# Optimization experiments

Measured on AMD Instinct MI355X. Metric: run time of the kernel, lower is better.

## Reference

```python
import jax, jax.numpy as jnp
import numpy as np

NEG_SLOPE = 0.2  # DenseGATConv default negative_slope


def _add_self_loops(adj):
    n = adj.shape[-1]
    idx = jnp.arange(n)
    return adj.at[:, idx, idx].set(1.0)


def dense_gat_conv(x, adj, W, att_src, att_dst, bias, concat):
    """PyG DenseGATConv forward (eval mode, add_loop=True).
    x: [B,N,F], adj: [B,N,N] (0/1), W: [F,H*C], att_*: [H,C], bias: [H*C] or [C]."""
    B, N, _ = x.shape
    H, C = att_src.shape
    h = (x @ W).reshape(B, N, H, C)                     # projected features
    a_src = jnp.einsum('bnhc,hc->bnh', h, att_src)      # [B,N,H]
    a_dst = jnp.einsum('bnhc,hc->bnh', h, att_dst)      # [B,N,H]
    # alpha[b,i,j,h] = a_src[b,j,h] + a_dst[b,i,h]
    alpha = a_src[:, None, :, :] + a_dst[:, :, None, :]  # [B,N,N,H]
    alpha = jax.nn.leaky_relu(alpha, NEG_SLOPE)
    adj = _add_self_loops(adj)
    alpha = jnp.where(adj[..., None] == 0, -jnp.inf, alpha)
    alpha = jax.nn.softmax(alpha, axis=2)               # softmax over sources j
    out = jnp.einsum('bijh,bjhc->bihc', alpha, h)       # [B,N,H,C]
    out = out.reshape(B, N, H * C) if concat else out.mean(axis=2)
    return out + bias


def setup_inputs() -> dict:
    key = jax.random.key(0)
    ks = jax.random.split(key, 10)
    B, N, F, H, C, NC = 1, 4096, 512, 8, 64, 16
    x = jax.random.normal(ks[0], (B, N, F), dtype=jnp.float32)
    adj = (jax.random.uniform(ks[1], (B, N, N)) < 0.01).astype(jnp.float32)
    s1 = 1.0 / np.sqrt(F)
    s2 = 1.0 / np.sqrt(H * C)
    return {
        'x': x,
        'adj': adj,
        'W1': jax.random.normal(ks[2], (F, H * C), dtype=jnp.float32) * s1,
        'att_src1': jax.random.normal(ks[3], (H, C), dtype=jnp.float32) * s1,
        'att_dst1': jax.random.normal(ks[4], (H, C), dtype=jnp.float32) * s1,
        'b1': jnp.zeros((H * C,), dtype=jnp.float32),
        'W2': jax.random.normal(ks[5], (H * C, NC), dtype=jnp.float32) * s2,
        'att_src2': jax.random.normal(ks[6], (1, NC), dtype=jnp.float32) * s2,
        'att_dst2': jax.random.normal(ks[7], (1, NC), dtype=jnp.float32) * s2,
        'b2': jnp.zeros((NC,), dtype=jnp.float32),
    }


def reference(x, adj, W1, att_src1, att_dst1, b1, W2, att_src2, att_dst2, b2):
    # eval mode: all dropout(p=0.6) layers are identity
    h = dense_gat_conv(x, adj, W1, att_src1, att_dst1, b1, concat=True)
    h = jax.nn.elu(h)
    out = dense_gat_conv(h, adj, W2, att_src2, att_dst2, b2, concat=False)
    return out
```

## Files before the change

### kernel.cpp

```cpp
#include <hip/hip_runtime.h>
#include <hip/hip_bf16.h>
#include <hip/hip_fp16.h>

#define N_NODES 4096
#define F_IN    512
#define HC      512
#define H_HEADS 8
#define C_DIM   64
#define NCLS    16
#define CAP     192
#define NEG_SLOPE 0.2f

typedef __bf16 bf16x8 __attribute__((ext_vector_type(8)));
typedef float  f32x4  __attribute__((ext_vector_type(4)));
typedef unsigned short us8 __attribute__((ext_vector_type(8)));


#define XBLKS 1024
#define WBLKS 64

__global__ __launch_bounds__(256) void k_prep(const float* __restrict__ x,
                                              const float* __restrict__ W,
                                              const float* __restrict__ adj,
                                              ushort* __restrict__ xhi,
                                              ushort* __restrict__ xlo,
                                              ushort* __restrict__ whiT,
                                              ushort* __restrict__ wloT,
                                              int* __restrict__ row_cnt,
                                              int* __restrict__ col_idx) {
    __shared__ float tile[64][65];
    __shared__ int cnt_s;
    int b = blockIdx.x;
    int t = threadIdx.x;
    if (b < XBLKS) {
        int tid = b * 256 + t;
        int rg = tid >> 9;
        rg = tid >> 10;
        int c  = tid & 1023;
        int kb = c >> 6;
        int l  = c & 63;
        int row = rg * 16 + (l & 15);
        int kbase = kb * 32 + (l >> 4) * 8;
        const float* src = &x[(size_t)row * F_IN + kbase];
        float4 v0 = *(const float4*)&src[0];
        float4 v1 = *(const float4*)&src[4];
        float f[8] = {v0.x, v0.y, v0.z, v0.w, v1.x, v1.y, v1.z, v1.w};
        us8 hv, lv;
#pragma unroll
        for (int u = 0; u < 8; ++u) {
            __bf16 h = (__bf16)f[u];
            __bf16 lo_ = (__bf16)(f[u] - (float)h);
            hv[u] = __builtin_bit_cast(unsigned short, h);
            lv[u] = __builtin_bit_cast(unsigned short, lo_);
        }
        *(us8*)&xhi[(size_t)tid * 8] = hv;
        *(us8*)&xlo[(size_t)tid * 8] = lv;
    } else if (b < XBLKS + WBLKS) {
        int bb = b - XBLKS;
        int n0 = (bb & 7) * 64, k0 = (bb >> 3) * 64;
#pragma unroll
        for (int i = 0; i < 4; ++i) {
            int r = i * 16 + (t >> 4);
            int c = (t & 15) * 4;
            *(float4*)&tile[r][c] = *(const float4*)&W[(size_t)(k0 + r) * HC + n0 + c];
        }
        __syncthreads();
        int rg_local = t >> 6;
        int l = t & 63;
        int n_local = rg_local * 16 + (l & 15);
#pragma unroll
        for (int kb_local = 0; kb_local < 2; ++kb_local) {
            int k_local = kb_local * 32 + (l >> 4) * 8;
            us8 hv, lv;
#pragma unroll
            for (int u = 0; u < 8; ++u) {
                float f = tile[k_local + u][n_local];
                __bf16 h = (__bf16)f;
                __bf16 lo_ = (__bf16)(f - (float)h);
                hv[u] = __builtin_bit_cast(unsigned short, h);
                lv[u] = __builtin_bit_cast(unsigned short, lo_);
            }
            int rg = (n0 >> 4) + rg_local;
            int kb = (k0 >> 5) + kb_local;
            size_t off = ((size_t)(rg * 16 + kb) * 64 + l) * 8;
            *(us8*)&whiT[off] = hv;
            *(us8*)&wloT[off] = lv;
        }
    } else {
        int i = b - (XBLKS + WBLKS);
        if (t == 0) cnt_s = 0;
        __syncthreads();
        const float4* row = (const float4*)(adj + (size_t)i * N_NODES);
        int* cols = col_idx + (size_t)i * CAP;
#pragma unroll
        for (int it = 0; it < 4; ++it) {
            int idx4 = it * 256 + t;
            float4 v = row[idx4];
            int j0 = idx4 * 4;
            if (v.x != 0.f && j0 + 0 != i) { int p = atomicAdd(&cnt_s, 1); if (p < CAP - 1) cols[p] = j0 + 0; }
            if (v.y != 0.f && j0 + 1 != i) { int p = atomicAdd(&cnt_s, 1); if (p < CAP - 1) cols[p] = j0 + 1; }
            if (v.z != 0.f && j0 + 2 != i) { int p = atomicAdd(&cnt_s, 1); if (p < CAP - 1) cols[p] = j0 + 2; }
            if (v.w != 0.f && j0 + 3 != i) { int p = atomicAdd(&cnt_s, 1); if (p < CAP - 1) cols[p] = j0 + 3; }
        }
        __syncthreads();
        if (t == 0) {
            int p = min(cnt_s, CAP - 1);
            cols[p] = i;
            row_cnt[i] = p + 1;
        }
    }
}

__global__ __launch_bounds__(256) void k_gemm1(const ushort* __restrict__ Ahi,
                                               const ushort* __restrict__ Alo,
                                               const ushort* __restrict__ Bhi,
                                               const ushort* __restrict__ Blo,
                                               const float* __restrict__ att_src,
                                               const float* __restrict__ att_dst,
                                               __half* __restrict__ C,
                                               float* __restrict__ a_src,
                                               float* __restrict__ a_dst) {
    __shared__ __align__(16) ushort smem[4][2048];
    __shared__ float s_s[2][64], s_d[2][64];
    int t = threadIdx.x;
    int w = t >> 6, lane = t & 63;
    int n0 = blockIdx.x * 64;
    int m0 = blockIdx.y * 64;
    const ushort* src = (w == 0) ? Ahi : (w == 1) ? Alo : (w == 2) ? Bhi : Blo;
    int rg0 = ((w < 2) ? m0 : n0) >> 4;
    int mw = (w & 1) * 32, nw = (w >> 1) * 32;
    f32x4 acc[2][2] = {};
    for (int kb = 0; kb < 16; ++kb) {
#pragma unroll
        for (int g = 0; g < 4; ++g) {
            const ushort* gp = src + ((size_t)((rg0 + g) * 16 + kb) * 64 + lane) * 8;
            __builtin_amdgcn_global_load_lds(
                (const __attribute__((address_space(1))) void*)gp,
                (__attribute__((address_space(3))) void*)&smem[w][g * 512],
                16, 0, 0);
        }
        __syncthreads();
        bf16x8 ahi[2], alo[2], bhi[2], blo[2];
#pragma unroll
        for (int mi = 0; mi < 2; ++mi) {
            int g = (mw >> 4) + mi;
            ahi[mi] = __builtin_bit_cast(bf16x8, *(const us8*)&smem[0][g * 512 + lane * 8]);
            alo[mi] = __builtin_bit_cast(bf16x8, *(const us8*)&smem[1][g * 512 + lane * 8]);
        }
#pragma unroll
        for (int ni = 0; ni < 2; ++ni) {
            int g = (nw >> 4) + ni;
            bhi[ni] = __builtin_bit_cast(bf16x8, *(const us8*)&smem[2][g * 512 + lane * 8]);
            blo[ni] = __builtin_bit_cast(bf16x8, *(const us8*)&smem[3][g * 512 + lane * 8]);
        }
#pragma unroll
        for (int mi = 0; mi < 2; ++mi)
#pragma unroll
            for (int ni = 0; ni < 2; ++ni) {
                acc[mi][ni] = __builtin_amdgcn_mfma_f32_16x16x32_bf16(ahi[mi], bhi[ni], acc[mi][ni], 0, 0, 0);
                acc[mi][ni] = __builtin_amdgcn_mfma_f32_16x16x32_bf16(alo[mi], bhi[ni], acc[mi][ni], 0, 0, 0);
                acc[mi][ni] = __builtin_amdgcn_mfma_f32_16x16x32_bf16(ahi[mi], blo[ni], acc[mi][ni], 0, 0, 0);
            }
        __syncthreads();
    }
    int r0 = (lane >> 4) * 4;
    int cn = lane & 15;
    float as0 = att_src[n0 + nw + cn],      as1 = att_src[n0 + nw + 16 + cn];
    float ad0 = att_dst[n0 + nw + cn],      ad1 = att_dst[n0 + nw + 16 + cn];
#pragma unroll
    for (int mi = 0; mi < 2; ++mi)
#pragma unroll
        for (int r = 0; r < 4; ++r) {
            float ps = acc[mi][0][r] * as0 + acc[mi][1][r] * as1;
            float pd = acc[mi][0][r] * ad0 + acc[mi][1][r] * ad1;
#pragma unroll
            for (int o = 1; o < 16; o <<= 1) {
                ps += __shfl_xor(ps, o, 64);
                pd += __shfl_xor(pd, o, 64);
            }
            if (cn == 0) {
                int row = mw + mi * 16 + r0 + r;
                s_s[w >> 1][row] = ps;
                s_d[w >> 1][row] = pd;
            }
        }
#pragma unroll
    for (int mi = 0; mi < 2; ++mi)
#pragma unroll
        for (int ni = 0; ni < 2; ++ni) {
            size_t base = (size_t)(m0 + mw + mi * 16 + r0) * HC + (n0 + nw + ni * 16 + cn);
#pragma unroll
            for (int r = 0; r < 4; ++r)
                C[base + (size_t)r * HC] = __float2half(acc[mi][ni][r]);
        }
    __syncthreads();
    if (t < 64) {
        a_src[(m0 + t) * H_HEADS + blockIdx.x] = s_s[0][t] + s_s[1][t];
        a_dst[(m0 + t) * H_HEADS + blockIdx.x] = s_d[0][t] + s_d[1][t];
    }
}

__global__ __launch_bounds__(256) void k_agg1(const __half* __restrict__ hf,
                                              const float* __restrict__ a_src,
                                              const float* __restrict__ a_dst,
                                              const int* __restrict__ row_cnt,
                                              const int* __restrict__ col_idx,
                                              const float* __restrict__ b1,
                                              __half* __restrict__ elu1) {
    int i = blockIdx.x;
    int t = threadIdx.x;
    __shared__ float wL[CAP][H_HEADS];
    __shared__ int   colL[CAP];
    __shared__ float denom[H_HEADS];
    __shared__ float ad[H_HEADS];
    int cnt = row_cnt[i];
    if (t < H_HEADS) ad[t] = a_dst[i * H_HEADS + t];
    for (int j = t; j < cnt; j += 256) colL[j] = col_idx[(size_t)i * CAP + j];
    __syncthreads();
    for (int idx = t; idx < cnt * H_HEADS; idx += 256) {
        int j = idx >> 3, h = idx & 7;
        float l = a_src[colL[j] * H_HEADS + h] + ad[h];
        l = (l > 0.f) ? l : NEG_SLOPE * l;
        wL[j][h] = __expf(l);
    }
    __syncthreads();
    {
        int h = t >> 5, l32 = t & 31;
        float s = 0.f;
        for (int j = l32; j < cnt; j += 32) s += wL[j][h];
#pragma unroll
        for (int o = 16; o > 0; o >>= 1) s += __shfl_down(s, o, 32);
        if (l32 == 0) denom[h] = s;
    }
    __syncthreads();
    int e = t * 2;
    int h = e >> 6;
    float ax = 0.f, ay = 0.f;
    int j = 0;
    for (; j + 4 <= cnt; j += 4) {
        int c0 = colL[j], c1 = colL[j + 1], c2 = colL[j + 2], c3 = colL[j + 3];
        float2 v0 = __half22float2(*(const __half2*)&hf[(size_t)c0 * HC + e]);
        float2 v1 = __half22float2(*(const __half2*)&hf[(size_t)c1 * HC + e]);
        float2 v2 = __half22float2(*(const __half2*)&hf[(size_t)c2 * HC + e]);
        float2 v3 = __half22float2(*(const __half2*)&hf[(size_t)c3 * HC + e]);
        float w0 = wL[j][h], w1 = wL[j + 1][h], w2 = wL[j + 2][h], w3 = wL[j + 3][h];
        ax += w0 * v0.x + w1 * v1.x + w2 * v2.x + w3 * v3.x;
        ay += w0 * v0.y + w1 * v1.y + w2 * v2.y + w3 * v3.y;
    }
    for (; j < cnt; ++j) {
        int c0 = colL[j];
        float2 v0 = __half22float2(*(const __half2*)&hf[(size_t)c0 * HC + e]);
        float w0 = wL[j][h];
        ax += w0 * v0.x;
        ay += w0 * v0.y;
    }
    float inv = 1.f / denom[h];
    float o0 = ax * inv + b1[e];
    float o1 = ay * inv + b1[e + 1];
    o0 = (o0 > 0.f) ? o0 : (__expf(o0) - 1.f);
    o1 = (o1 > 0.f) ? o1 : (__expf(o1) - 1.f);
    *(__half2*)&elu1[(size_t)i * HC + e] = __floats2half2_rn(o0, o1);
}

__global__ __launch_bounds__(256) void k_gemm2(const __half* __restrict__ elu1,
                                               const float* __restrict__ W2,
                                               const float* __restrict__ att_src2,
                                               const float* __restrict__ att_dst2,
                                               float* __restrict__ h2,
                                               float* __restrict__ a_src2,
                                               float* __restrict__ a_dst2) {
    __shared__ float W2s[HC * NCLS];
    __shared__ float h2s[16][NCLS];
    int t = threadIdx.x;
    int n0 = blockIdx.x * 16;
#pragma unroll
    for (int u = 0; u < 8; ++u) {
        int idx = (u * 256 + t) * 4;
        *(float4*)&W2s[idx] = *(const float4*)&W2[idx];
    }
    __syncthreads();
    int nl = t >> 4, c = t & 15;
    const __half2* row = (const __half2*)(elu1 + (size_t)(n0 + nl) * HC);
    float acc = 0.f;
    for (int k = 0; k < HC; k += 4) {
        float2 v0 = __half22float2(row[k >> 1]);
        float2 v1 = __half22float2(row[(k >> 1) + 1]);
        acc += v0.x * W2s[(k + 0) * NCLS + c] + v0.y * W2s[(k + 1) * NCLS + c]
             + v1.x * W2s[(k + 2) * NCLS + c] + v1.y * W2s[(k + 3) * NCLS + c];
    }
    h2[(size_t)(n0 + nl) * NCLS + c] = acc;
    h2s[nl][c] = acc;
    __syncthreads();
    if (t < 16) {
        float s = 0.f, d = 0.f;
#pragma unroll
        for (int cc = 0; cc < NCLS; ++cc) {
            s += h2s[t][cc] * att_src2[cc];
            d += h2s[t][cc] * att_dst2[cc];
        }
        a_src2[n0 + t] = s;
        a_dst2[n0 + t] = d;
    }
}

__global__ __launch_bounds__(256) void k_agg2(const float* __restrict__ h2,
                                              const float* __restrict__ a_src2,
                                              const float* __restrict__ a_dst2,
                                              const int* __restrict__ row_cnt,
                                              const int* __restrict__ col_idx,
                                              const float* __restrict__ b2,
                                              float* __restrict__ out) {
    int t = threadIdx.x;
    int w = t >> 6, lane = t & 63;
    int i = blockIdx.x * 4 + w;
    __shared__ float ew[4][CAP];
    __shared__ int   colL[4][CAP];
    int cnt = row_cnt[i];
    float adi = a_dst2[i];
    float sum = 0.f;
    for (int j = lane; j < cnt; j += 64) {
        int col = col_idx[(size_t)i * CAP + j];
        colL[w][j] = col;
        float l = a_src2[col] + adi;
        l = (l > 0.f) ? l : NEG_SLOPE * l;
        float e = __expf(l);
        ew[w][j] = e;
        sum += e;
    }
#pragma unroll
    for (int o = 32; o > 0; o >>= 1) sum += __shfl_xor(sum, o, 64);
    int q = lane >> 4, c = lane & 15;
    float acc = 0.f;
    for (int j = q; j < cnt; j += 4)
        acc += ew[w][j] * h2[(size_t)colL[w][j] * NCLS + c];
    acc += __shfl_down(acc, 32, 64);
    acc += __shfl_down(acc, 16, 64);
    if (lane < NCLS)
        out[(size_t)i * NCLS + lane] = acc / sum + b2[lane];
}

extern "C" void kernel_launch(void* const* d_in, const int* in_sizes, int n_in,
                              void* d_out, int out_size, void* d_ws, size_t ws_size,
                              hipStream_t stream) {
    const float* x        = (const float*)d_in[0];
    const float* adj      = (const float*)d_in[1];
    const float* W1       = (const float*)d_in[2];
    const float* att_src1 = (const float*)d_in[3];
    const float* att_dst1 = (const float*)d_in[4];
    const float* b1       = (const float*)d_in[5];
    const float* W2       = (const float*)d_in[6];
    const float* att_src2 = (const float*)d_in[7];
    const float* att_dst2 = (const float*)d_in[8];
    const float* b2       = (const float*)d_in[9];
    float* out = (float*)d_out;

    char* ws = (char*)d_ws;
    int*    row_cnt = (int*)ws;     ws += (size_t)N_NODES * 4;
    int*    col_idx = (int*)ws;     ws += (size_t)N_NODES * CAP * 4;
    __half* h1f     = (__half*)ws;  ws += (size_t)N_NODES * HC * 2;
    float*  a_src   = (float*)ws;   ws += (size_t)N_NODES * H_HEADS * 4;
    float*  a_dst   = (float*)ws;   ws += (size_t)N_NODES * H_HEADS * 4;
    __half* elu1    = (__half*)ws;  ws += (size_t)N_NODES * HC * 2;
    float*  h2      = (float*)ws;   ws += (size_t)N_NODES * NCLS * 4;
    float*  as2     = (float*)ws;   ws += (size_t)N_NODES * 4;
    float*  ad2     = (float*)ws;   ws += (size_t)N_NODES * 4;
    ushort* x_hi    = (ushort*)ws;  ws += (size_t)N_NODES * F_IN * 2;
    ushort* x_lo    = (ushort*)ws;  ws += (size_t)N_NODES * F_IN * 2;
    ushort* w_hiT   = (ushort*)ws;  ws += (size_t)F_IN * HC * 2;
    ushort* w_loT   = (ushort*)ws;  ws += (size_t)F_IN * HC * 2;

    hipLaunchKernelGGL(k_prep, dim3(XBLKS + WBLKS + N_NODES), dim3(256), 0, stream,
                       x, W1, adj, x_hi, x_lo, w_hiT, w_loT, row_cnt, col_idx);
    hipLaunchKernelGGL(k_gemm1, dim3(HC / 64, N_NODES / 64), dim3(256), 0, stream,
                       x_hi, x_lo, w_hiT, w_loT, att_src1, att_dst1, h1f, a_src, a_dst);
    hipLaunchKernelGGL(k_agg1, dim3(N_NODES), dim3(256), 0, stream,
                       h1f, a_src, a_dst, row_cnt, col_idx, b1, elu1);
    hipLaunchKernelGGL(k_gemm2, dim3(N_NODES / 16), dim3(256), 0, stream,
                       elu1, W2, att_src2, att_dst2, h2, as2, ad2);
    hipLaunchKernelGGL(k_agg2, dim3(N_NODES / 4), dim3(256), 0, stream,
                       h2, as2, ad2, row_cnt, col_idx, b2, out);
}
```

Baseline: 165.5 us.

## Fuse second-layer projection into aggregation and overlap adjacency scan with GEMM1

Moves the adjacency-to-CSR scan out of the prep kernel into extra blocks of the first GEMM launch, so the adjacency read runs alongside the projection GEMM. Fuses the second linear projection and its attention logits into the first aggregation kernel. Each node's ELU output now stays in shared memory and is multiplied by W2 there, which removes the elu1 round trip through global memory and one kernel launch. In exchange, each aggregation block reads W2 directly from global memory (cached) and adds two block barriers and a small reduction.

```diff
diff --git a/kernel.cpp b/kernel.cpp
--- a/kernel.cpp
+++ b/kernel.cpp
@@ -18,24 +18,20 @@
 
 #define XBLKS 1024
 #define WBLKS 64
-
-__global__ __launch_bounds__(256) void k_prep(const float* __restrict__ x,
-                                              const float* __restrict__ W,
-                                              const float* __restrict__ adj,
-                                              ushort* __restrict__ xhi,
-                                              ushort* __restrict__ xlo,
-                                              ushort* __restrict__ whiT,
-                                              ushort* __restrict__ wloT,
-                                              int* __restrict__ row_cnt,
-                                              int* __restrict__ col_idx) {
+#define GBLKS 512
+
+__global__ __launch_bounds__(256) void k_split(const float* __restrict__ x,
+                                               const float* __restrict__ W,
+                                               ushort* __restrict__ xhi,
+                                               ushort* __restrict__ xlo,
+                                               ushort* __restrict__ whiT,
+                                               ushort* __restrict__ wloT) {
     __shared__ float tile[64][65];
-    __shared__ int cnt_s;
     int b = blockIdx.x;
     int t = threadIdx.x;
     if (b < XBLKS) {
         int tid = b * 256 + t;
-        int rg = tid >> 9;
-        rg = tid >> 10;
+        int rg = tid >> 10;
         int c  = tid & 1023;
         int kb = c >> 6;
         int l  = c & 63;
@@ -55,7 +51,7 @@
         }
         *(us8*)&xhi[(size_t)tid * 8] = hv;
         *(us8*)&xlo[(size_t)tid * 8] = lv;
-    } else if (b < XBLKS + WBLKS) {
+    } else {
         int bb = b - XBLKS;
         int n0 = (bb & 7) * 64, k0 = (bb >> 3) * 64;
 #pragma unroll
@@ -86,8 +82,28 @@
             *(us8*)&whiT[off] = hv;
             *(us8*)&wloT[off] = lv;
         }
-    } else {
-        int i = b - (XBLKS + WBLKS);
+    }
+}
+
+__global__ __launch_bounds__(256) void k_gemm1(const ushort* __restrict__ Ahi,
+                                               const ushort* __restrict__ Alo,
+                                               const ushort* __restrict__ Bhi,
+                                               const ushort* __restrict__ Blo,
+                                               const float* __restrict__ att_src,
+                                               const float* __restrict__ att_dst,
+                                               const float* __restrict__ adj,
+                                               __half* __restrict__ C,
+                                               float* __restrict__ a_src,
+                                               float* __restrict__ a_dst,
+                                               int* __restrict__ row_cnt,
+                                               int* __restrict__ col_idx) {
+    __shared__ __align__(16) ushort smem[4][2048];
+    __shared__ float s_s[2][64], s_d[2][64];
+    __shared__ int cnt_s;
+    int b = blockIdx.x;
+    int t = threadIdx.x;
+    if (b >= GBLKS) {
+        int i = b - GBLKS;
         if (t == 0) cnt_s = 0;
         __syncthreads();
         const float4* row = (const float4*)(adj + (size_t)i * N_NODES);
@@ -108,24 +124,12 @@
             cols[p] = i;
             row_cnt[i] = p + 1;
         }
-    }
-}
-
-__global__ __launch_bounds__(256) void k_gemm1(const ushort* __restrict__ Ahi,
-                                               const ushort* __restrict__ Alo,
-                                               const ushort* __restrict__ Bhi,
-                                               const ushort* __restrict__ Blo,
-                                               const float* __restrict__ att_src,
-                                               const float* __restrict__ att_dst,
-                                               __half* __restrict__ C,
-                                               float* __restrict__ a_src,
-                                               float* __restrict__ a_dst) {
-    __shared__ __align__(16) ushort smem[4][2048];
-    __shared__ float s_s[2][64], s_d[2][64];
-    int t = threadIdx.x;
+        return;
+    }
     int w = t >> 6, lane = t & 63;
-    int n0 = blockIdx.x * 64;
-    int m0 = blockIdx.y * 64;
+    int head = b & 7;
+    int n0 = head * 64;
+    int m0 = (b >> 3) * 64;
     const ushort* src = (w == 0) ? Ahi : (w == 1) ? Alo : (w == 2) ? Bhi : Blo;
     int rg0 = ((w < 2) ? m0 : n0) >> 4;
     int mw = (w & 1) * 32, nw = (w >> 1) * 32;
@@ -195,8 +199,8 @@
         }
     __syncthreads();
     if (t < 64) {
-        a_src[(m0 + t) * H_HEADS + blockIdx.x] = s_s[0][t] + s_s[1][t];
-        a_dst[(m0 + t) * H_HEADS + blockIdx.x] = s_d[0][t] + s_d[1][t];
+        a_src[(m0 + t) * H_HEADS + head] = s_s[0][t] + s_s[1][t];
+        a_dst[(m0 + t) * H_HEADS + head] = s_d[0][t] + s_d[1][t];
     }
 }
 
@@ -206,13 +210,20 @@
                                               const int* __restrict__ row_cnt,
                                               const int* __restrict__ col_idx,
                                               const float* __restrict__ b1,
-                                              __half* __restrict__ elu1) {
+                                              const float* __restrict__ W2,
+                                              const float* __restrict__ att_src2,
+                                              const float* __restrict__ att_dst2,
+                                              float* __restrict__ h2,
+                                              float* __restrict__ a_src2,
+                                              float* __restrict__ a_dst2) {
     int i = blockIdx.x;
     int t = threadIdx.x;
     __shared__ float wL[CAP][H_HEADS];
     __shared__ int   colL[CAP];
     __shared__ float denom[H_HEADS];
     __shared__ float ad[H_HEADS];
+    __shared__ float elu_s[HC];
+    __shared__ float part[16][17];
     int cnt = row_cnt[i];
     if (t < H_HEADS) ad[t] = a_dst[i * H_HEADS + t];
     for (int j = t; j < cnt; j += 256) colL[j] = col_idx[(size_t)i * CAP + j];
@@ -259,47 +270,29 @@
     float o1 = ay * inv + b1[e + 1];
     o0 = (o0 > 0.f) ? o0 : (__expf(o0) - 1.f);
     o1 = (o1 > 0.f) ? o1 : (__expf(o1) - 1.f);
-    *(__half2*)&elu1[(size_t)i * HC + e] = __floats2half2_rn(o0, o1);
-}
-
-__global__ __launch_bounds__(256) void k_gemm2(const __half* __restrict__ elu1,
-                                               const float* __restrict__ W2,
-                                               const float* __restrict__ att_src2,
-                                               const float* __restrict__ att_dst2,
-                                               float* __restrict__ h2,
-                                               float* __restrict__ a_src2,
-                                               float* __restrict__ a_dst2) {
-    __shared__ float W2s[HC * NCLS];
-    __shared__ float h2s[16][NCLS];
-    int t = threadIdx.x;
-    int n0 = blockIdx.x * 16;
-#pragma unroll
-    for (int u = 0; u < 8; ++u) {
-        int idx = (u * 256 + t) * 4;
-        *(float4*)&W2s[idx] = *(const float4*)&W2[idx];
-    }
-    __syncthreads();
-    int nl = t >> 4, c = t & 15;
-    const __half2* row = (const __half2*)(elu1 + (size_t)(n0 + nl) * HC);
-    float acc = 0.f;
-    for (int k = 0; k < HC; k += 4) {
-        float2 v0 = __half22float2(row[k >> 1]);
-        float2 v1 = __half22float2(row[(k >> 1) + 1]);
-        acc += v0.x * W2s[(k + 0) * NCLS + c] + v0.y * W2s[(k + 1) * NCLS + c]
-             + v1.x * W2s[(k + 2) * NCLS + c] + v1.y * W2s[(k + 3) * NCLS + c];
-    }
-    h2[(size_t)(n0 + nl) * NCLS + c] = acc;
-    h2s[nl][c] = acc;
+    elu_s[e]     = o0;
+    elu_s[e + 1] = o1;
+    __syncthreads();
+    int kg = t >> 4, c = t & 15;
+    float p = 0.f;
+    const float* w2p = W2 + (size_t)kg * 32 * NCLS + c;
+    const float* es  = &elu_s[kg * 32];
+#pragma unroll 8
+    for (int kk = 0; kk < 32; ++kk) p += es[kk] * w2p[kk * NCLS];
+    part[kg][c] = p;
     __syncthreads();
     if (t < 16) {
-        float s = 0.f, d = 0.f;
-#pragma unroll
-        for (int cc = 0; cc < NCLS; ++cc) {
-            s += h2s[t][cc] * att_src2[cc];
-            d += h2s[t][cc] * att_dst2[cc];
-        }
-        a_src2[n0 + t] = s;
-        a_dst2[n0 + t] = d;
+        float s = 0.f;
+#pragma unroll
+        for (int r = 0; r < 16; ++r) s += part[r][t];
+        h2[(size_t)i * NCLS + t] = s;
+        float vs = s * att_src2[t], vd = s * att_dst2[t];
+#pragma unroll
+        for (int o = 8; o > 0; o >>= 1) {
+            vs += __shfl_xor(vs, o, 64);
+            vd += __shfl_xor(vd, o, 64);
+        }
+        if (t == 0) { a_src2[i] = vs; a_dst2[i] = vd; }
     }
 }
 
@@ -360,7 +353,6 @@
     __half* h1f     = (__half*)ws;  ws += (size_t)N_NODES * HC * 2;
     float*  a_src   = (float*)ws;   ws += (size_t)N_NODES * H_HEADS * 4;
     float*  a_dst   = (float*)ws;   ws += (size_t)N_NODES * H_HEADS * 4;
-    __half* elu1    = (__half*)ws;  ws += (size_t)N_NODES * HC * 2;
     float*  h2      = (float*)ws;   ws += (size_t)N_NODES * NCLS * 4;
     float*  as2     = (float*)ws;   ws += (size_t)N_NODES * 4;
     float*  ad2     = (float*)ws;   ws += (size_t)N_NODES * 4;
@@ -369,14 +361,14 @@
     ushort* w_hiT   = (ushort*)ws;  ws += (size_t)F_IN * HC * 2;
     ushort* w_loT   = (ushort*)ws;  ws += (size_t)F_IN * HC * 2;
 
-    hipLaunchKernelGGL(k_prep, dim3(XBLKS + WBLKS + N_NODES), dim3(256), 0, stream,
-                       x, W1, adj, x_hi, x_lo, w_hiT, w_loT, row_cnt, col_idx);
-    hipLaunchKernelGGL(k_gemm1, dim3(HC / 64, N_NODES / 64), dim3(256), 0, stream,
-                       x_hi, x_lo, w_hiT, w_loT, att_src1, att_dst1, h1f, a_src, a_dst);
+    hipLaunchKernelGGL(k_split, dim3(XBLKS + WBLKS), dim3(256), 0, stream,
+                       x, W1, x_hi, x_lo, w_hiT, w_loT);
+    hipLaunchKernelGGL(k_gemm1, dim3(GBLKS + N_NODES), dim3(256), 0, stream,
+                       x_hi, x_lo, w_hiT, w_loT, att_src1, att_dst1, adj,
+                       h1f, a_src, a_dst, row_cnt, col_idx);
     hipLaunchKernelGGL(k_agg1, dim3(N_NODES), dim3(256), 0, stream,
-                       h1f, a_src, a_dst, row_cnt, col_idx, b1, elu1);
-    hipLaunchKernelGGL(k_gemm2, dim3(N_NODES / 16), dim3(256), 0, stream,
-                       elu1, W2, att_src2, att_dst2, h2, as2, ad2);
+                       h1f, a_src, a_dst, row_cnt, col_idx, b1,
+                       W2, att_src2, att_dst2, h2, as2, ad2);
     hipLaunchKernelGGL(k_agg2, dim3(N_NODES / 4), dim3(256), 0, stream,
                        h2, as2, ad2, row_cnt, col_idx, b2, out);
 }
```

Result: faster. 154.6 us (-6.6%).
